# Kernel tuning notes

Hardware: AMD Instinct MI355X
Metric: run time of the kernel (lower is better)

The kernel has to match this reference:

```python
import jax, jax.numpy as jnp
import numpy as np


def setup_inputs() -> dict:
    key = jax.random.key(0)
    k1, k2, k3 = jax.random.split(key, 3)
    B, C, H, W = 8, 256, 128, 128
    Ck, Cv = 256, 256
    scale = 1.0 / np.sqrt(C)  # ~kaiming-style init for 1x1 conv
    return {
        "x": jax.random.normal(k1, (B, C, H, W), dtype=jnp.float32),
        "Wk": jax.random.normal(k2, (Ck, C), dtype=jnp.float32) * scale,
        "bk": jnp.zeros((Ck,), dtype=jnp.float32),
        "Wv": jax.random.normal(k3, (Cv, C), dtype=jnp.float32) * scale,
        "bv": jnp.zeros((Cv,), dtype=jnp.float32),
    }


def reference(x, Wk, bk, Wv, bv):
    # x: [B, C, H, W]; 1x1 convs are channel GEMMs.
    B, C, H, W = x.shape
    xf = x.reshape(B, C, H * W)                      # [B, C, N]
    keys = jnp.einsum("kc,bcn->bkn", Wk, xf) + bk[None, :, None]   # [B, Ck, N]
    keys = jax.nn.softmax(keys, axis=2)              # softmax over spatial N
    values = jnp.einsum("vc,bcn->bvn", Wv, xf) + bv[None, :, None]  # [B, Cv, N]
    context = jnp.einsum("bkn,bvn->bkv", keys, values)  # [B, Ck, Cv]
    return context
```

## Files before the change

kernel.cpp:

```cpp
#include <hip/hip_runtime.h>

typedef unsigned short u16;
typedef __attribute__((ext_vector_type(8))) short bf16x8;
typedef __attribute__((ext_vector_type(4))) float f32x4;

#define CDIM 256
#define NDIM 16384
#define NBATCH 8
#define TLEN 64
#define SCHUNK 16
#define NC (NDIM / SCHUNK)

#define WS_WK  0u
#define WS_WV  131072u
#define WS_CTX 262144u
#define WS_L   2359296u
#define WS_END 2367488u

__device__ __forceinline__ u16 f2bf(float f) {
  union { float f; unsigned u; } v; v.f = f;
  return (u16)((v.u + 0x7fffu + ((v.u >> 16) & 1u)) >> 16);
}

__global__ void prep_weights(const float* __restrict__ Wk, const float* __restrict__ Wv,
                             u16* __restrict__ wkb, u16* __restrict__ wvb) {
  int i = blockIdx.x * 256 + threadIdx.x;
  wkb[i] = f2bf(Wk[i]);
  wvb[i] = f2bf(Wv[i]);
}

__global__ __launch_bounds__(256, 2) void attn_main(
    const float* __restrict__ x, const u16* __restrict__ wkb, const u16* __restrict__ wvb,
    float* __restrict__ ctx_acc, float* __restrict__ l_acc) {
  __shared__ u16 xs[32][TLEN][8];
  __shared__ u16 ps[8][128][8];
  __shared__ u16 vs[8][128][8];

  const int bid = blockIdx.x;
  const int kt = (bid >> 1) & 1;
  const int vt = bid & 1;
  const int chunk = (bid >> 2) & (SCHUNK - 1);
  const int b = bid >> 6;

  const int tid = threadIdx.x;
  const int wave = tid >> 6;
  const int lane = tid & 63;
  const int l15 = lane & 15;
  const int l4 = lane >> 4;
  const int wr = wave >> 1;
  const int wc = wave & 1;

  f32x4 cacc[4][4] = {};
  float lreg[2][4] = {};

  const float* xb = x + (size_t)b * CDIM * NDIM + (size_t)chunk * NC;
  const int krow0 = kt * 128 + wave * 32 + l15;
  const int vrow0 = vt * 128 + wave * 32 + l15;

  for (int t = 0; t < NC / TLEN; ++t) {
    const float* xt = xb + t * TLEN;

    {
      const int c0 = tid >> 4;
      const int nq = (tid & 15) * 4;
      #pragma unroll
      for (int p = 0; p < 16; ++p) {
        const int c = c0 + p * 16;
        const float4 v4 = *reinterpret_cast<const float4*>(&xt[(size_t)c * NDIM + nq]);
        xs[c >> 3][nq + 0][c & 7] = f2bf(v4.x);
        xs[c >> 3][nq + 1][c & 7] = f2bf(v4.y);
        xs[c >> 3][nq + 2][c & 7] = f2bf(v4.z);
        xs[c >> 3][nq + 3][c & 7] = f2bf(v4.w);
      }
    }
    __syncthreads();

    f32x4 sacc[2][4] = {};
    #pragma unroll
    for (int kk = 0; kk < 8; ++kk) {
      const int c0 = kk * 32 + l4 * 8;
      const bf16x8 a0 = *reinterpret_cast<const bf16x8*>(&wkb[krow0 * 256 + c0]);
      const bf16x8 a1 = *reinterpret_cast<const bf16x8*>(&wkb[(krow0 + 16) * 256 + c0]);
      #pragma unroll
      for (int cf = 0; cf < 4; ++cf) {
        const int n = cf * 16 + l15;
        const bf16x8 bx = *reinterpret_cast<const bf16x8*>(&xs[c0 >> 3][n][0]);
        sacc[0][cf] = __builtin_amdgcn_mfma_f32_16x16x32_bf16(a0, bx, sacc[0][cf], 0, 0, 0);
        sacc[1][cf] = __builtin_amdgcn_mfma_f32_16x16x32_bf16(a1, bx, sacc[1][cf], 0, 0, 0);
      }
    }

    #pragma unroll
    for (int rf = 0; rf < 2; ++rf) {
      float rs[4] = {0.f, 0.f, 0.f, 0.f};
      #pragma unroll
      for (int cf = 0; cf < 4; ++cf) {
        const int n = cf * 16 + l15;
        #pragma unroll
        for (int r = 0; r < 4; ++r) {
          const float pe = __expf(sacc[rf][cf][r]);
          rs[r] += pe;
          ps[n >> 3][wave * 32 + rf * 16 + l4 * 4 + r][n & 7] = f2bf(pe);
        }
      }
      #pragma unroll
      for (int r = 0; r < 4; ++r) {
        float s2 = rs[r];
        s2 += __shfl_xor(s2, 1);
        s2 += __shfl_xor(s2, 2);
        s2 += __shfl_xor(s2, 4);
        s2 += __shfl_xor(s2, 8);
        lreg[rf][r] += s2;
      }
    }

    f32x4 vacc[2][4] = {};
    #pragma unroll
    for (int kk = 0; kk < 8; ++kk) {
      const int c0 = kk * 32 + l4 * 8;
      const bf16x8 a0 = *reinterpret_cast<const bf16x8*>(&wvb[vrow0 * 256 + c0]);
      const bf16x8 a1 = *reinterpret_cast<const bf16x8*>(&wvb[(vrow0 + 16) * 256 + c0]);
      #pragma unroll
      for (int cf = 0; cf < 4; ++cf) {
        const int n = cf * 16 + l15;
        const bf16x8 bx = *reinterpret_cast<const bf16x8*>(&xs[c0 >> 3][n][0]);
        vacc[0][cf] = __builtin_amdgcn_mfma_f32_16x16x32_bf16(a0, bx, vacc[0][cf], 0, 0, 0);
        vacc[1][cf] = __builtin_amdgcn_mfma_f32_16x16x32_bf16(a1, bx, vacc[1][cf], 0, 0, 0);
      }
    }
    #pragma unroll
    for (int rf = 0; rf < 2; ++rf)
      #pragma unroll
      for (int cf = 0; cf < 4; ++cf) {
        const int n = cf * 16 + l15;
        #pragma unroll
        for (int r = 0; r < 4; ++r)
          vs[n >> 3][wave * 32 + rf * 16 + l4 * 4 + r][n & 7] = f2bf(vacc[rf][cf][r]);
      }
    __syncthreads();

    #pragma unroll
    for (int kk = 0; kk < 2; ++kk) {
      const int n0 = kk * 32 + l4 * 8;
      bf16x8 bfr[4];
      #pragma unroll
      for (int cf = 0; cf < 4; ++cf)
        bfr[cf] = *reinterpret_cast<const bf16x8*>(&vs[n0 >> 3][wc * 64 + cf * 16 + l15][0]);
      #pragma unroll
      for (int af = 0; af < 4; ++af) {
        const bf16x8 pa = *reinterpret_cast<const bf16x8*>(&ps[n0 >> 3][wr * 64 + af * 16 + l15][0]);
        #pragma unroll
        for (int cf = 0; cf < 4; ++cf)
          cacc[af][cf] = __builtin_amdgcn_mfma_f32_16x16x32_bf16(pa, bfr[cf], cacc[af][cf], 0, 0, 0);
      }
    }
    __syncthreads();
  }

  float* ctxb = ctx_acc + (size_t)b * 256 * 256;
  #pragma unroll
  for (int af = 0; af < 4; ++af) {
    const int kq = kt * 128 + wr * 64 + af * 16 + l4 * 4;
    #pragma unroll
    for (int cf = 0; cf < 4; ++cf) {
      const int vg = vt * 128 + wc * 64 + cf * 16 + l15;
      #pragma unroll
      for (int r = 0; r < 4; ++r)
        atomicAdd(&ctxb[(kq + r) * 256 + vg], cacc[af][cf][r]);
    }
  }
  if (vt == 0 && l15 == 0) {
    #pragma unroll
    for (int rf = 0; rf < 2; ++rf)
      #pragma unroll
      for (int r = 0; r < 4; ++r)
        atomicAdd(&l_acc[b * 256 + kt * 128 + wave * 32 + rf * 16 + l4 * 4 + r], lreg[rf][r]);
  }
}

__global__ void finalize_kernel(const float* __restrict__ ctx_acc, const float* __restrict__ l_acc,
                                const float* __restrict__ bv, float* __restrict__ out) {
  int idx = blockIdx.x * 256 + threadIdx.x;
  out[idx] = ctx_acc[idx] / l_acc[idx >> 8] + bv[idx & 255];
}

extern "C" void kernel_launch(void* const* d_in, const int* in_sizes, int n_in,
                              void* d_out, int out_size, void* d_ws, size_t ws_size,
                              hipStream_t stream) {
  const float* x  = (const float*)d_in[0];
  const float* Wk = (const float*)d_in[1];
  const float* Wv = (const float*)d_in[3];
  const float* bv = (const float*)d_in[4];
  float* out = (float*)d_out;
  char* ws = (char*)d_ws;

  u16* wkb = (u16*)(ws + WS_WK);
  u16* wvb = (u16*)(ws + WS_WV);
  float* ctx = (float*)(ws + WS_CTX);
  float* l   = (float*)(ws + WS_L);

  hipMemsetAsync(ws + WS_CTX, 0, WS_END - WS_CTX, stream);
  prep_weights<<<256, 256, 0, stream>>>(Wk, Wv, wkb, wvb);
  attn_main<<<NBATCH * SCHUNK * 4, 256, 0, stream>>>(x, wkb, wvb, ctx, l);
  finalize_kernel<<<2048, 256, 0, stream>>>(ctx, l, bv, out);
}
```

Baseline: 521.6 us.

## Restructure attention kernel: full-K/V per block, 32x32 MFMA, swizzled LDS, prefetch

Each block now computes all 256 key and value channels for its spatial chunk with 512 threads, instead of splitting into 2x2 k/v tiles. This removes the redundant recomputation of the key GEMM and softmax exp across the old vt split, and of the value GEMM across the old kt split. The kernel switches to 32x32x16 bf16 MFMA, uses XOR-swizzled LDS layouts with vectorized packed stores, and register-prefetches the next x tile to overlap global loads with compute. It also lowers the block count (256 blocks) and raises register and LDS pressure, which may reduce occupancy.

```diff
diff --git a/kernel.cpp b/kernel.cpp
--- a/kernel.cpp
+++ b/kernel.cpp
@@ -1,15 +1,17 @@
 #include <hip/hip_runtime.h>
 
 typedef unsigned short u16;
+typedef unsigned int u32;
 typedef __attribute__((ext_vector_type(8))) short bf16x8;
-typedef __attribute__((ext_vector_type(4))) float f32x4;
+typedef __attribute__((ext_vector_type(16))) float f32x16;
 
 #define CDIM 256
 #define NDIM 16384
 #define NBATCH 8
+#define NCHUNK 32
+#define CHUNK_N 512
 #define TLEN 64
-#define SCHUNK 16
-#define NC (NDIM / SCHUNK)
+#define NTILES 8
 
 #define WS_WK  0u
 #define WS_WV  131072u
@@ -21,6 +23,10 @@
   union { float f; unsigned u; } v; v.f = f;
   return (u16)((v.u + 0x7fffu + ((v.u >> 16) & 1u)) >> 16);
 }
+__device__ __forceinline__ u32 pack2(float lo, float hi) {
+  return (u32)f2bf(lo) | ((u32)f2bf(hi) << 16);
+}
+__device__ __forceinline__ int swz(int off) { return off ^ (((off >> 7) & 7) << 4); }
 
 __global__ void prep_weights(const float* __restrict__ Wk, const float* __restrict__ Wv,
                              u16* __restrict__ wkb, u16* __restrict__ wvb) {
@@ -29,152 +35,140 @@
   wvb[i] = f2bf(Wv[i]);
 }
 
-__global__ __launch_bounds__(256, 2) void attn_main(
+__device__ __forceinline__ void pack_store(const f32x16& g0, const f32x16& g1,
+                                           char* base, int row, int h) {
+  #pragma unroll
+  for (int nt = 0; nt < 2; ++nt) {
+    const f32x16& g = nt ? g1 : g0;
+    #pragma unroll
+    for (int bq = 0; bq < 4; ++bq) {
+      uint2 w;
+      w.x = pack2(g[4 * bq + 0], g[4 * bq + 1]);
+      w.y = pack2(g[4 * bq + 2], g[4 * bq + 3]);
+      const int n = nt * 32 + 8 * bq + 4 * h;
+      *reinterpret_cast<uint2*>(base + swz(row * 128 + n * 2)) = w;
+    }
+  }
+}
+
+__global__ __launch_bounds__(512) void attn_main(
     const float* __restrict__ x, const u16* __restrict__ wkb, const u16* __restrict__ wvb,
     float* __restrict__ ctx_acc, float* __restrict__ l_acc) {
-  __shared__ u16 xs[32][TLEN][8];
-  __shared__ u16 ps[8][128][8];
-  __shared__ u16 vs[8][128][8];
+  __shared__ u16 xs[16384];
+  __shared__ u16 ps[16384];
+  __shared__ u16 vs[16384];
 
   const int bid = blockIdx.x;
-  const int kt = (bid >> 1) & 1;
-  const int vt = bid & 1;
-  const int chunk = (bid >> 2) & (SCHUNK - 1);
-  const int b = bid >> 6;
-
+  const int chunk = bid & (NCHUNK - 1);
+  const int b = bid >> 5;
   const int tid = threadIdx.x;
-  const int wave = tid >> 6;
+  const int wv = tid >> 6;
   const int lane = tid & 63;
-  const int l15 = lane & 15;
-  const int l4 = lane >> 4;
-  const int wr = wave >> 1;
-  const int wc = wave & 1;
-
-  f32x4 cacc[4][4] = {};
-  float lreg[2][4] = {};
-
-  const float* xb = x + (size_t)b * CDIM * NDIM + (size_t)chunk * NC;
-  const int krow0 = kt * 128 + wave * 32 + l15;
-  const int vrow0 = vt * 128 + wave * 32 + l15;
-
-  for (int t = 0; t < NC / TLEN; ++t) {
-    const float* xt = xb + t * TLEN;
-
+  const int l31 = lane & 31;
+  const int h = lane >> 5;
+
+  const float* xb = x + (size_t)b * CDIM * NDIM + chunk * CHUNK_N;
+
+  const int so = tid >> 4;
+  const int sc = so * 8;
+  const int sn = (tid & 15) * 4;
+
+  const u16* wkp = wkb + (wv * 32 + l31) * 256 + h * 8;
+  const u16* wvp = wvb + (wv * 32 + l31) * 256 + h * 8;
+
+  f32x16 acc[8] = {};
+  float lsum = 0.f;
+
+  char* xsb = (char*)&xs[0];
+  char* psb = (char*)&ps[0];
+  char* vsb = (char*)&vs[0];
+
+  float4 pf[8];
+
+  #pragma unroll
+  for (int p = 0; p < 8; ++p)
+    pf[p] = *reinterpret_cast<const float4*>(xb + (size_t)(sc + p) * NDIM + sn);
+
+  for (int t = 0; t < NTILES; ++t) {
     {
-      const int c0 = tid >> 4;
-      const int nq = (tid & 15) * 4;
+      uint4 w0, w1, w2, w3;
+      w0.x = pack2(pf[0].x, pf[1].x); w0.y = pack2(pf[2].x, pf[3].x); w0.z = pack2(pf[4].x, pf[5].x); w0.w = pack2(pf[6].x, pf[7].x);
+      w1.x = pack2(pf[0].y, pf[1].y); w1.y = pack2(pf[2].y, pf[3].y); w1.z = pack2(pf[4].y, pf[5].y); w1.w = pack2(pf[6].y, pf[7].y);
+      w2.x = pack2(pf[0].z, pf[1].z); w2.y = pack2(pf[2].z, pf[3].z); w2.z = pack2(pf[4].z, pf[5].z); w2.w = pack2(pf[6].z, pf[7].z);
+      w3.x = pack2(pf[0].w, pf[1].w); w3.y = pack2(pf[2].w, pf[3].w); w3.z = pack2(pf[4].w, pf[5].w); w3.w = pack2(pf[6].w, pf[7].w);
+      *reinterpret_cast<uint4*>(xsb + swz(so * 1024 + (sn + 0) * 16)) = w0;
+      *reinterpret_cast<uint4*>(xsb + swz(so * 1024 + (sn + 1) * 16)) = w1;
+      *reinterpret_cast<uint4*>(xsb + swz(so * 1024 + (sn + 2) * 16)) = w2;
+      *reinterpret_cast<uint4*>(xsb + swz(so * 1024 + (sn + 3) * 16)) = w3;
+    }
+    __syncthreads();
+
+    if (t < NTILES - 1) {
       #pragma unroll
-      for (int p = 0; p < 16; ++p) {
-        const int c = c0 + p * 16;
-        const float4 v4 = *reinterpret_cast<const float4*>(&xt[(size_t)c * NDIM + nq]);
-        xs[c >> 3][nq + 0][c & 7] = f2bf(v4.x);
-        xs[c >> 3][nq + 1][c & 7] = f2bf(v4.y);
-        xs[c >> 3][nq + 2][c & 7] = f2bf(v4.z);
-        xs[c >> 3][nq + 3][c & 7] = f2bf(v4.w);
+      for (int p = 0; p < 8; ++p)
+        pf[p] = *reinterpret_cast<const float4*>(xb + (size_t)(sc + p) * NDIM + (t + 1) * TLEN + sn);
+    }
+
+    f32x16 g0 = {}, g1 = {};
+    #pragma unroll
+    for (int kk = 0; kk < 16; ++kk) {
+      const int oct = kk * 2 + h;
+      bf16x8 a0 = *reinterpret_cast<const bf16x8*>(xsb + swz(oct * 1024 + l31 * 16));
+      bf16x8 a1 = *reinterpret_cast<const bf16x8*>(xsb + swz(oct * 1024 + (32 + l31) * 16));
+      bf16x8 bk = *reinterpret_cast<const bf16x8*>(wkp + kk * 16);
+      g0 = __builtin_amdgcn_mfma_f32_32x32x16_bf16(a0, bk, g0, 0, 0, 0);
+      g1 = __builtin_amdgcn_mfma_f32_32x32x16_bf16(a1, bk, g1, 0, 0, 0);
+    }
+
+    float ls = 0.f;
+    #pragma unroll
+    for (int r = 0; r < 16; ++r) { g0[r] = __expf(g0[r]); ls += g0[r]; }
+    #pragma unroll
+    for (int r = 0; r < 16; ++r) { g1[r] = __expf(g1[r]); ls += g1[r]; }
+    lsum += ls;
+    pack_store(g0, g1, psb, wv * 32 + l31, h);
+
+    g0 = {}; g1 = {};
+    #pragma unroll
+    for (int kk = 0; kk < 16; ++kk) {
+      const int oct = kk * 2 + h;
+      bf16x8 a0 = *reinterpret_cast<const bf16x8*>(xsb + swz(oct * 1024 + l31 * 16));
+      bf16x8 a1 = *reinterpret_cast<const bf16x8*>(xsb + swz(oct * 1024 + (32 + l31) * 16));
+      bf16x8 bw = *reinterpret_cast<const bf16x8*>(wvp + kk * 16);
+      g0 = __builtin_amdgcn_mfma_f32_32x32x16_bf16(a0, bw, g0, 0, 0, 0);
+      g1 = __builtin_amdgcn_mfma_f32_32x32x16_bf16(a1, bw, g1, 0, 0, 0);
+    }
+    pack_store(g0, g1, vsb, wv * 32 + l31, h);
+
+    __syncthreads();
+
+    bf16x8 paf[4];
+    #pragma unroll
+    for (int kk = 0; kk < 4; ++kk)
+      paf[kk] = *reinterpret_cast<const bf16x8*>(
+          psb + swz((wv * 32 + l31) * 128 + (kk * 16 + h * 8) * 2));
+    #pragma unroll
+    for (int vt = 0; vt < 8; ++vt) {
+      #pragma unroll
+      for (int kk = 0; kk < 4; ++kk) {
+        bf16x8 bvf = *reinterpret_cast<const bf16x8*>(
+            vsb + swz((vt * 32 + l31) * 128 + (kk * 16 + h * 8) * 2));
+        acc[vt] = __builtin_amdgcn_mfma_f32_32x32x16_bf16(paf[kk], bvf, acc[vt], 0, 0, 0);
       }
     }
-    __syncthreads();
-
-    f32x4 sacc[2][4] = {};
-    #pragma unroll
-    for (int kk = 0; kk < 8; ++kk) {
-      const int c0 = kk * 32 + l4 * 8;
-      const bf16x8 a0 = *reinterpret_cast<const bf16x8*>(&wkb[krow0 * 256 + c0]);
-      const bf16x8 a1 = *reinterpret_cast<const bf16x8*>(&wkb[(krow0 + 16) * 256 + c0]);
-      #pragma unroll
-      for (int cf = 0; cf < 4; ++cf) {
-        const int n = cf * 16 + l15;
-        const bf16x8 bx = *reinterpret_cast<const bf16x8*>(&xs[c0 >> 3][n][0]);
-        sacc[0][cf] = __builtin_amdgcn_mfma_f32_16x16x32_bf16(a0, bx, sacc[0][cf], 0, 0, 0);
-        sacc[1][cf] = __builtin_amdgcn_mfma_f32_16x16x32_bf16(a1, bx, sacc[1][cf], 0, 0, 0);
-      }
-    }
-
-    #pragma unroll
-    for (int rf = 0; rf < 2; ++rf) {
-      float rs[4] = {0.f, 0.f, 0.f, 0.f};
-      #pragma unroll
-      for (int cf = 0; cf < 4; ++cf) {
-        const int n = cf * 16 + l15;
-        #pragma unroll
-        for (int r = 0; r < 4; ++r) {
-          const float pe = __expf(sacc[rf][cf][r]);
-          rs[r] += pe;
-          ps[n >> 3][wave * 32 + rf * 16 + l4 * 4 + r][n & 7] = f2bf(pe);
-        }
-      }
-      #pragma unroll
-      for (int r = 0; r < 4; ++r) {
-        float s2 = rs[r];
-        s2 += __shfl_xor(s2, 1);
-        s2 += __shfl_xor(s2, 2);
-        s2 += __shfl_xor(s2, 4);
-        s2 += __shfl_xor(s2, 8);
-        lreg[rf][r] += s2;
-      }
-    }
-
-    f32x4 vacc[2][4] = {};
-    #pragma unroll
-    for (int kk = 0; kk < 8; ++kk) {
-      const int c0 = kk * 32 + l4 * 8;
-      const bf16x8 a0 = *reinterpret_cast<const bf16x8*>(&wvb[vrow0 * 256 + c0]);
-      const bf16x8 a1 = *reinterpret_cast<const bf16x8*>(&wvb[(vrow0 + 16) * 256 + c0]);
-      #pragma unroll
-      for (int cf = 0; cf < 4; ++cf) {
-        const int n = cf * 16 + l15;
-        const bf16x8 bx = *reinterpret_cast<const bf16x8*>(&xs[c0 >> 3][n][0]);
-        vacc[0][cf] = __builtin_amdgcn_mfma_f32_16x16x32_bf16(a0, bx, vacc[0][cf], 0, 0, 0);
-        vacc[1][cf] = __builtin_amdgcn_mfma_f32_16x16x32_bf16(a1, bx, vacc[1][cf], 0, 0, 0);
-      }
-    }
-    #pragma unroll
-    for (int rf = 0; rf < 2; ++rf)
-      #pragma unroll
-      for (int cf = 0; cf < 4; ++cf) {
-        const int n = cf * 16 + l15;
-        #pragma unroll
-        for (int r = 0; r < 4; ++r)
-          vs[n >> 3][wave * 32 + rf * 16 + l4 * 4 + r][n & 7] = f2bf(vacc[rf][cf][r]);
-      }
-    __syncthreads();
-
-    #pragma unroll
-    for (int kk = 0; kk < 2; ++kk) {
-      const int n0 = kk * 32 + l4 * 8;
-      bf16x8 bfr[4];
-      #pragma unroll
-      for (int cf = 0; cf < 4; ++cf)
-        bfr[cf] = *reinterpret_cast<const bf16x8*>(&vs[n0 >> 3][wc * 64 + cf * 16 + l15][0]);
-      #pragma unroll
-      for (int af = 0; af < 4; ++af) {
-        const bf16x8 pa = *reinterpret_cast<const bf16x8*>(&ps[n0 >> 3][wr * 64 + af * 16 + l15][0]);
-        #pragma unroll
-        for (int cf = 0; cf < 4; ++cf)
-          cacc[af][cf] = __builtin_amdgcn_mfma_f32_16x16x32_bf16(pa, bfr[cf], cacc[af][cf], 0, 0, 0);
-      }
-    }
-    __syncthreads();
   }
 
-  float* ctxb = ctx_acc + (size_t)b * 256 * 256;
+  lsum += __shfl_xor(lsum, 32);
+  if (h == 0) atomicAdd(&l_acc[b * 256 + wv * 32 + l31], lsum);
+
+  float* ctxb = ctx_acc + (size_t)b * 65536;
   #pragma unroll
-  for (int af = 0; af < 4; ++af) {
-    const int kq = kt * 128 + wr * 64 + af * 16 + l4 * 4;
-    #pragma unroll
-    for (int cf = 0; cf < 4; ++cf) {
-      const int vg = vt * 128 + wc * 64 + cf * 16 + l15;
-      #pragma unroll
-      for (int r = 0; r < 4; ++r)
-        atomicAdd(&ctxb[(kq + r) * 256 + vg], cacc[af][cf][r]);
-    }
-  }
-  if (vt == 0 && l15 == 0) {
-    #pragma unroll
-    for (int rf = 0; rf < 2; ++rf)
-      #pragma unroll
-      for (int r = 0; r < 4; ++r)
-        atomicAdd(&l_acc[b * 256 + kt * 128 + wave * 32 + rf * 16 + l4 * 4 + r], lreg[rf][r]);
+  for (int vt = 0; vt < 8; ++vt) {
+    #pragma unroll
+    for (int r = 0; r < 16; ++r) {
+      const int k = wv * 32 + (r & 3) + 8 * (r >> 2) + 4 * h;
+      atomicAdd(&ctxb[k * 256 + vt * 32 + l31], acc[vt][r]);
+    }
   }
 }
 
@@ -201,6 +195,6 @@
 
   hipMemsetAsync(ws + WS_CTX, 0, WS_END - WS_CTX, stream);
   prep_weights<<<256, 256, 0, stream>>>(Wk, Wv, wkb, wvb);
-  attn_main<<<NBATCH * SCHUNK * 4, 256, 0, stream>>>(x, wkb, wvb, ctx, l);
+  attn_main<<<NBATCH * NCHUNK, 512, 0, stream>>>(x, wkb, wvb, ctx, l);
   finalize_kernel<<<2048, 256, 0, stream>>>(ctx, l, bv, out);
 }
```

Result: slower. 549.5 us (+5.4%).
